# Optimization experiments

Measured on AMD Instinct MI355X. Metric: run time of the kernel, lower is better.

Reference implementation:

```python
import jax, jax.numpy as jnp
import numpy as np
from jax import lax

SCALES = [0.5, 1, 2]


def resize_bilinear_ac(x, oh, ow):
    """F.interpolate(mode='bilinear', align_corners=True) for NCHW x."""
    B, C, H, W = x.shape
    def coords(n_in, n_out):
        c = jnp.linspace(0.0, n_in - 1.0, n_out).astype(x.dtype)
        i0 = jnp.clip(jnp.floor(c).astype(jnp.int32), 0, n_in - 1)
        i1 = jnp.minimum(i0 + 1, n_in - 1)
        return i0, i1, c - i0.astype(x.dtype)
    y0, y1, wy = coords(H, oh)
    x0, x1, wx = coords(W, ow)
    top = x[:, :, y0, :] * (1 - wy)[:, None] + x[:, :, y1, :] * wy[:, None]
    return top[:, :, :, x0] * (1 - wx) + top[:, :, :, x1] * wx


def interpolate4d(t, oh, ow):
    """Geometry.interpolate4d: bilinear resize of both spatial pairs of [b,h1,w1,h2,w2]."""
    b, h1, w1, h2, w2 = t.shape
    t = t.reshape(b, h1, w1, h2 * w2).transpose(0, 3, 1, 2)
    t = resize_bilinear_ac(t, oh, ow)            # [b, h2*w2, oh, ow]
    t = t.reshape(b, h2, w2, oh * ow).transpose(0, 3, 1, 2)
    t = resize_bilinear_ac(t, oh, ow)            # [b, oh*ow, oh, ow]
    return t.reshape(b, oh, ow, oh, ow)


def conv2d_same(x, w):
    return lax.conv_general_dilated(x, w, (1, 1), [(1, 1), (1, 1)],
                                    dimension_numbers=('NCHW', 'OIHW', 'NCHW'))


def conv3d_same(x, w, p):
    return lax.conv_general_dilated(x, w, (1, 1, 1), [(p, p)] * 3,
                                    dimension_numbers=('NCDHW', 'OIDHW', 'NCDHW'))


def fast4d(corr, kernel, bias=None):
    """4D conv (stride 1, same zero-padding) via per-slice 3D convs, mirroring chm.fast4d.
    corr: [b, ci, sh, sw, th, tw]; kernel: [co, ci, k, k, k, k]."""
    b, ci, sh, sw, th, tw = corr.shape
    co, k = kernel.shape[0], kernel.shape[2]
    p = k // 2
    x = corr.transpose(0, 2, 1, 3, 4, 5).reshape(b * sh, ci, sw, th, tw)
    out = jnp.zeros((b, co, sh, sw, th, tw), corr.dtype)
    for pidx in range(k):
        ic = conv3d_same(x, kernel[:, :, pidx], p)
        ic = ic.reshape(b, sh, co, sw, th, tw).transpose(0, 2, 1, 3, 4, 5)
        a0, a1 = max(p - pidx, 0), min(sh, sh + p - pidx)
        s0, s1 = max(pidx - p, 0), min(sh, sh + pidx - p)
        out = out.at[:, :, a0:a1].add(ic[:, :, s0:s1])
    if bias is not None:
        out = out + bias.reshape(1, co, 1, 1, 1, 1)
    return out


def chm6d(corr, kernel):
    """6D conv with kernel (K,K,kk,kk,kk,kk), same zero-padding, no bias (chm.fast6d).
    corr: [b, 1, S, S, h, w, h, w]; kernel: [1, 1, K, K, kk, kk, kk, kk]."""
    b, _, S, _, h, w, _, _ = corr.shape
    K, kk = kernel.shape[2], kernel.shape[4]
    pk = K // 2
    x = corr.transpose(0, 2, 3, 1, 4, 5, 6, 7).reshape(b * S * S, 1, h, w, h, w)
    ker = kernel.reshape(1, K * K, kk, kk, kk, kk).swapaxes(0, 1)  # [K*K, 1, kk...]
    y = fast4d(x, ker).reshape(b, S, S, K * K, h, w, h, w)
    yp = jnp.pad(y, ((0, 0), (pk, pk), (pk, pk), (0, 0), (0, 0), (0, 0), (0, 0), (0, 0)))
    out = jnp.zeros((b, S, S, h, w, h, w), corr.dtype)
    for ki in range(K):
        for kj in range(K):
            out = out + yp[:, ki:ki + S, kj:kj + S, ki * K + kj]
    return out[:, None]


def mutual_nn_filter(cm):
    smax = jnp.max(cm, axis=2, keepdims=True)
    tmax = jnp.max(cm, axis=1, keepdims=True)
    smax = jnp.where(smax == 0, 1e-30, smax)
    tmax = jnp.where(tmax == 0, 1e-30, tmax)
    return cm * ((cm / smax) * (cm / tmax))


def build_correlation6d(src_feat, trg_feat, conv_ws):
    bsz, _, side, _ = src_feat.shape
    sfs, tfs = [], []
    for scale, w in zip(SCALES, conv_ws):
        s = int(np.floor(scale * side))
        sfs.append(conv2d_same(resize_bilinear_ac(src_feat, s, s), w))
        tfs.append(conv2d_same(resize_bilinear_ac(trg_feat, s, s), w))
    corr6d = []
    for sf in sfs:
        ch, ss = sf.shape[1], sf.shape[-1]
        sv = sf.reshape(bsz, ch, ss * ss).transpose(0, 2, 1)   # [b, ss^2, ch]
        sn = jnp.linalg.norm(sv, axis=2, keepdims=True)
        for tf in tfs:
            ts = tf.shape[-1]
            tv = tf.reshape(bsz, ch, ts * ts)                  # [b, ch, ts^2]
            tn = jnp.linalg.norm(tv, axis=1, keepdims=True)
            c = jnp.einsum('bsc,bct->bst', sv, tv) / (sn * tn)
            corr6d.append(interpolate4d(c.reshape(bsz, ss, ss, ts, ts), side, side))
    corr = jnp.stack(corr6d).reshape(3, 3, bsz, side, side, side, side)
    corr = corr.transpose(2, 0, 1, 3, 4, 5, 6)                 # [b, 3, 3, s, s, s, s]
    return jnp.maximum(corr, 0.0)


def chm_forward(src_feat, trg_feat, w0, w1, w2, k6, k4, b4):
    bsz, _, side, _ = src_feat.shape
    corr = build_correlation6d(src_feat, trg_feat, (w0, w1, w2))[:, None]
    corr = jax.nn.sigmoid(chm6d(corr, k6))                     # [b,1,3,3,h,w,h,w]
    h = w = side
    corr = corr.reshape(bsz, -1, h, w, h, w).max(axis=1)       # max over 9 scale pairs
    corr = interpolate4d(corr, 2 * h, 2 * w)[:, None]          # [b,1,2h,2w,2h,2w]
    corr = jax.nn.softplus(fast4d(corr, k4, b4)[:, 0])
    n = corr.shape[-1] ** 2
    return mutual_nn_filter(corr.reshape(bsz, n, n))


def setup_inputs() -> dict:
    key = jax.random.key(0)
    ks = jax.random.split(key, 8)
    b, fd, side = 4, 1024, 16
    w_std = 0.02  # ~kaiming for 3x3 conv with fan_in 1024*9
    return {
        'src_feat': jax.random.normal(ks[0], (b, fd, side, side), jnp.float32),
        'trg_feat': jax.random.normal(ks[1], (b, fd, side, side), jnp.float32),
        'conv_w0': jax.random.normal(ks[2], (fd // 4, fd, 3, 3), jnp.float32) * w_std,
        'conv_w1': jax.random.normal(ks[3], (fd // 4, fd, 3, 3), jnp.float32) * w_std,
        'conv_w2': jax.random.normal(ks[4], (fd // 4, fd, 3, 3), jnp.float32) * w_std,
        'chm6d_w': jax.random.normal(ks[5], (1, 1, 3, 3, 5, 5, 5, 5), jnp.float32) * 0.05,
        'chm4d_w': jax.random.normal(ks[6], (1, 1, 5, 5, 5, 5), jnp.float32) * 0.05,
        'chm4d_b': jnp.zeros((1,), jnp.float32),
    }


def reference(src_feat, trg_feat, conv_w0, conv_w1, conv_w2, chm6d_w, chm4d_w, chm4d_b):
    return chm_forward(src_feat, trg_feat, conv_w0, conv_w1, conv_w2, chm6d_w, chm4d_w, chm4d_b)
```

## Files before the change

kernel.cpp:

```cpp
#include <hip/hip_runtime.h>
#include <cstdint>
#include <cstddef>


#define DEVFN __device__ __forceinline__

typedef __attribute__((ext_vector_type(8))) short short8v;
typedef __attribute__((ext_vector_type(4))) float f32x4;
typedef unsigned int u32;

DEVFN void gl_lds16(const void* g, void* l){
  __builtin_amdgcn_global_load_lds(
      (const __attribute__((address_space(1))) u32*)g,
      (__attribute__((address_space(3))) u32*)l, 16, 0, 0);
}

constexpr size_t OFF_WB    = 0;
constexpr size_t OFF_P8    = 3538944;
constexpr size_t OFF_P16   = 3948544;
constexpr size_t OFF_P32   = 5275648;
constexpr size_t OFF_SF8   = 10010624;
constexpr size_t OFF_TF8   = 10076160;
constexpr size_t OFF_SF16  = 10141696;
constexpr size_t OFF_TF16  = 10403840;
constexpr size_t OFF_SF32  = 10665984;
constexpr size_t OFF_TF32  = 11714560;
constexpr size_t OFF_INVS  = 12763136;
constexpr size_t OFF_INVT  = 12768512;
constexpr size_t OFF_TMAX  = 12777984;
constexpr size_t OFF_CORR6 = 12782080;
constexpr size_t OFF_CMAXP = OFF_CORR6 + 2359296 + 128;
constexpr size_t OFF_WA    = OFF_CMAXP + 131072;
constexpr size_t OFF_PARTK = OFF_WA + 96128;
constexpr size_t OFF_SMAXP = OFF_PARTK + 2752512;
constexpr size_t OFF_WA4   = OFF_SMAXP + 16384;
constexpr size_t WS_FLOATS = OFF_WA4 + 12800;

__device__ constexpr size_t PAIR_OFF[9] = {
  OFF_WB + 0,       OFF_WB + 16384,   OFF_WB + 81920,
  OFF_WB + 344064,  OFF_WB + 409600,  OFF_WB + 671744,
  OFF_WB + 1720320, OFF_WB + 1982464, OFF_WB + 3031040 };
constexpr size_t OFF_CL    = 0;
constexpr size_t OFF_MAXED = 9437184;
constexpr size_t OFF_INT32 = 262144;
constexpr size_t OFF_FB    = OFF_PARTK;

__device__ constexpr int SSARR[3] = {8, 16, 32};
__device__ constexpr int PAIR_START[9] = {0,4,20,84,100,164,420,484,740};

DEVFN unsigned short f2bf(float f){
  unsigned int u = __float_as_uint(f);
  return (unsigned short)((u + 0x7fffu + ((u >> 16) & 1u)) >> 16);
}
DEVFN float bf2f(unsigned short u){
  return __uint_as_float(((unsigned int)u) << 16);
}

__global__ __launch_bounds__(256) void k_wpack(const float* __restrict__ w0,
                                               const float* __restrict__ w1,
                                               const float* __restrict__ w2,
                                               float* __restrict__ wsf){
  int bx = blockIdx.x;
  int scale = bx >> 8, cg = (bx >> 4) & 15, ig = bx & 15;
  const float* w = (scale==0) ? w0 : (scale==1 ? w1 : w2);
  const int t = threadIdx.x;
  __shared__ float sW[16*580];
  const float* src = w + (size_t)cg*16*9216 + (size_t)ig*576;
  for (int i=t; i<9216; i+=256){
    int co = i/576, r = i%576;
    sW[co*580 + r] = src[(size_t)co*9216 + r];
  }
  __syncthreads();
  unsigned short* ob = (unsigned short*)(wsf + OFF_WB) + (size_t)scale*2359296;
  for (int f=t; f<1152; f+=256){
    int tap = f/128, rem = f%128, kcl = rem>>6, l = rem&63;
    int kc = ig*2 + kcl;
    int co = l & 15;
    int ciL = kcl*32 + ((l>>4)&3)*8;
    unsigned short* o = ob + ((size_t)tap*32768 + (size_t)kc*1024 + (size_t)cg*64 + l)*8;
    #pragma unroll
    for (int i=0;i<8;i++)
      o[i] = f2bf(sW[co*580 + (ciL+i)*9 + tap]);
  }
}

__global__ void k_wa(const float* __restrict__ k6, float* __restrict__ wsf){
  int gid = blockIdx.x*256 + threadIdx.x;
  if (gid >= 24000) return;
  int tap = gid / 192, rem = gid % 192;
  int kc = rem / 64, l = rem % 64;
  int d = tap % 5, ac = tap / 5, a = ac / 5, c = ac % 5;
  int so = l & 15, k8 = (l >> 4) * 8;
  unsigned short* o = (unsigned short*)(wsf + OFF_WA) + (size_t)gid*8;
  #pragma unroll
  for (int i=0;i<8;i++){
    int kg = kc*32 + k8 + i;
    int e = kg >> 4, pr = kg & 15;
    float v = 0.f;
    if (so < 9 && pr < 9 && e < 5){
      int pi = pr/3, pj = pr%3, sio = so/3, sjo = so%3;
      int ki = pi - sio + 1, kj = pj - sjo + 1;
      if (ki>=0 && ki<=2 && kj>=0 && kj<=2)
        v = k6[(((((ki*3+kj)*5 + a)*5 + c)*5 + d)*5) + e];
    }
    o[i] = f2bf(v);
  }
}

__global__ void k_wa4(const float* __restrict__ k4, float* __restrict__ wsf){
  int gid = blockIdx.x*256 + threadIdx.x;
  if (gid >= 3200) return;
  int d = gid / 640, rem = gid % 640;
  int kc = rem / 64, l = rem % 64;
  int so = l & 15, soy = so >> 2, sox = so & 3;
  int e = kc >> 1;
  int pyw = 4*(kc & 1) + (l >> 4);
  unsigned short* o = (unsigned short*)(wsf + OFF_WA4) + (size_t)gid*8;
  #pragma unroll
  for (int i=0;i<8;i++){
    int a = pyw - soy, c = i - sox;
    float v = 0.f;
    if (a>=0 && a<=4 && c>=0 && c<=4)
      v = k4[((a*5 + c)*5 + d)*5 + e];
    o[i] = f2bf(v);
  }
}

__global__ __launch_bounds__(256) void k_inpack(const float* __restrict__ src,
                                                const float* __restrict__ trg,
                                                float* __restrict__ wsf){
  int bt = blockIdx.x >> 6, cg = blockIdx.x & 63;
  int chbase = cg*16;
  int t = threadIdx.x;
  __shared__ float sIn[16][257];
  const float* gin = ((bt>=4)? trg : src) + ((size_t)(bt&3)*1024 + chbase)*256;
  #pragma unroll
  for (int i=0;i<16;i++){
    int idx = t + i*256; int ch = idx>>8, pos = idx&255;
    sIn[ch][pos] = gin[(size_t)ch*256 + pos];
  }
  __syncthreads();
  int ch = t & 15, pw = t >> 4;
  #pragma unroll 1
  for (int s=0; s<3; s++){
    int S = SSARR[s], Sp = S+2, Sp2 = Sp*Sp;
    size_t poff = (s==0)?OFF_P8 : (s==1)?OFF_P16 : OFF_P32;
    unsigned short* o = (unsigned short*)(wsf + poff) + (size_t)bt*Sp2*1024 + chbase + ch;
    float rs = 15.f/(float)(S-1);
    for (int i = pw; i < Sp2; i += 16){
      int py = i / Sp, px = i % Sp;
      float v = 0.f;
      if (py>0 && py<Sp-1 && px>0 && px<Sp-1){
        float cy = (float)(py-1)*rs, cx = (float)(px-1)*rs;
        int y0 = (int)cy; if (y0>15) y0=15; int y1 = (y0+1<16)?y0+1:15; float fy = cy-(float)y0;
        int x0 = (int)cx; if (x0>15) x0=15; int x1 = (x0+1<16)?x0+1:15; float fx = cx-(float)x0;
        v = (1.f-fy)*((1.f-fx)*sIn[ch][y0*16+x0] + fx*sIn[ch][y0*16+x1])
          +       fy*((1.f-fx)*sIn[ch][y1*16+x0] + fx*sIn[ch][y1*16+x1]);
      }
      o[(size_t)i*1024] = f2bf(v);
    }
  }
}

__global__ __launch_bounds__(256) void k_conv_mfma(float* __restrict__ wsf){
  int bs = (blockIdx.x & 7)*84 + (blockIdx.x >> 3);
  const int ks = bs & 1;
  int bx = bs >> 1;
  int scale, bt, cot, post, S, lgS;
  if (bx < 256)      { scale=2; S=32; lgS=5; bt=bx>>5; cot=(bx>>4)&1; post=bx&15; }
  else if (bx < 320) { int r=bx-256; scale=1; S=16; lgS=4; bt=r>>3; cot=(r>>2)&1; post=r&3; }
  else               { int r=bx-320; scale=0; S=8;  lgS=3; bt=r>>1; cot=r&1; post=0; }
  const int Sp = S+2, N = S*S;
  const unsigned short* WbS = (const unsigned short*)(wsf + OFF_WB) + (size_t)scale*2359296;
  size_t poff = scale==0?OFF_P8: scale==1?OFF_P16:OFF_P32;
  const unsigned short* Pb = (const unsigned short*)(wsf + poff) + (size_t)bt*Sp*Sp*1024;
  size_t obase = (scale==2) ? (bt>=4?OFF_TF32:OFF_SF32)
               : (scale==1) ? (bt>=4?OFF_TF16:OFF_SF16)
                            : (bt>=4?OFF_TF8 :OFF_SF8);
  if (ks) obase += OFF_PARTK - OFF_SF8;
  float* outp = wsf + obase + (size_t)(bt&3)*256*N;

  const int t = threadIdx.x, l = t&63, w = t>>6, wm = w&1, wn = w>>1;
  const int nc_base = cot*8;
  const int pos0 = post*64;
  const int it0 = ks*72, it1 = it0 + 72;

  __shared__ __align__(16) unsigned short Ab[2][8192];
  __shared__ __align__(16) unsigned short Bb[2][4096];

  f32x4 acc[4][2];
  #pragma unroll
  for (int i=0;i<4;i++)
    #pragma unroll
    for (int j=0;j<2;j++) acc[i][j] = (f32x4){0.f,0.f,0.f,0.f};

  auto STAGE = [&](int buf, int it){
    int tap = it>>4, kq = it&15;
    int dy = tap/3, dx = tap - dy*3;
    #pragma unroll
    for (int j=0;j<4;++j){
      int c = w + j*4;
      int kc = c>>3, nc = c&7;
      const unsigned short* src =
        WbS + ((((size_t)tap*32 + kq*2 + kc)*16 + nc_base + nc)*64 + l)*8;
      gl_lds16(src, &Ab[buf][c*512]);
    }
    #pragma unroll
    for (int j=0;j<2;++j){
      int c = w + j*4;
      int kc = c>>2, np = c&3;
      int pos = pos0 + np*16 + (l&15);
      int y = pos>>lgS, x = pos&(S-1);
      int row = (y+dy)*Sp + (x+dx);
      int ci = kq*64 + kc*32 + ((l>>4)<<3);
      gl_lds16(Pb + (size_t)row*1024 + ci, &Bb[buf][c*512]);
    }
  };

  STAGE(0, it0);
  __syncthreads();
  int buf = 0;
  #pragma unroll 1
  for (int it=it0; it<it1; ++it){
    if (it+1 < it1) STAGE(buf^1, it+1);
    #pragma unroll
    for (int kc=0; kc<2; ++kc){
      short8v a0 = *(const short8v*)&Ab[buf][((kc*8 + wm*4 + 0)*64 + l)*8];
      short8v a1 = *(const short8v*)&Ab[buf][((kc*8 + wm*4 + 1)*64 + l)*8];
      short8v a2 = *(const short8v*)&Ab[buf][((kc*8 + wm*4 + 2)*64 + l)*8];
      short8v a3 = *(const short8v*)&Ab[buf][((kc*8 + wm*4 + 3)*64 + l)*8];
      short8v b0 = *(const short8v*)&Bb[buf][((kc*4 + wn*2 + 0)*64 + l)*8];
      short8v b1 = *(const short8v*)&Bb[buf][((kc*4 + wn*2 + 1)*64 + l)*8];
      acc[0][0] = __builtin_amdgcn_mfma_f32_16x16x32_bf16(a0, b0, acc[0][0], 0,0,0);
      acc[1][0] = __builtin_amdgcn_mfma_f32_16x16x32_bf16(a1, b0, acc[1][0], 0,0,0);
      acc[2][0] = __builtin_amdgcn_mfma_f32_16x16x32_bf16(a2, b0, acc[2][0], 0,0,0);
      acc[3][0] = __builtin_amdgcn_mfma_f32_16x16x32_bf16(a3, b0, acc[3][0], 0,0,0);
      acc[0][1] = __builtin_amdgcn_mfma_f32_16x16x32_bf16(a0, b1, acc[0][1], 0,0,0);
      acc[1][1] = __builtin_amdgcn_mfma_f32_16x16x32_bf16(a1, b1, acc[1][1], 0,0,0);
      acc[2][1] = __builtin_amdgcn_mfma_f32_16x16x32_bf16(a2, b1, acc[2][1], 0,0,0);
      acc[3][1] = __builtin_amdgcn_mfma_f32_16x16x32_bf16(a3, b1, acc[3][1], 0,0,0);
    }
    __syncthreads();
    buf ^= 1;
  }

  const int r0 = (l>>4)*4, cl = l&15;
  float* ob = outp + (size_t)(cot*128 + wm*64)*N + pos0 + wn*32 + cl;
  #pragma unroll
  for (int mf=0; mf<4; ++mf)
    #pragma unroll
    for (int nf=0; nf<2; ++nf){
      float* op = ob + (size_t)(mf*16 + r0)*N + nf*16;
      #pragma unroll
      for (int i=0;i<4;++i) op[(size_t)i*N] = acc[mf][nf][i];
    }
}

__global__ void k_combine(float* __restrict__ ws){
  int i = blockIdx.x*256 + threadIdx.x;
  ws[OFF_SF8 + i] += ws[OFF_PARTK + i];
}

__global__ __launch_bounds__(256) void k_fbpack(float* __restrict__ ws){
  int bx = blockIdx.x;
  int tsr = bx/84, r = bx%84;
  int s, b, chunk;
  if (r < 4)       { s=0; b=r;        chunk=0; }
  else if (r < 20) { s=1; int q=r-4;  b=q>>2; chunk=q&3; }
  else             { s=2; int q=r-20; b=q>>4; chunk=q&15; }
  int P = SSARR[s]*SSARR[s];
  size_t fbase = (s==0)? (tsr?OFF_TF8 :OFF_SF8)
               : (s==1)? (tsr?OFF_TF16:OFF_SF16)
                       : (tsr?OFF_TF32:OFF_SF32);
  const float* src = ws + fbase + (size_t)b*256*P;
  int pos0 = chunk*64;
  const int t = threadIdx.x;
  __shared__ float tile[64][260];
  for (int i=0;i<64;i++){
    int idx = t + i*256; int ch = idx>>6, pl = idx&63;
    tile[pl][ch] = src[(size_t)ch*P + pos0 + pl];
  }
  __syncthreads();
  int rowbase = tsr*5376 + (s==0?0: s==1?256:1280) + b*P + pos0;
  unsigned short* FB = (unsigned short*)(ws + OFF_FB);
  for (int i=0;i<64;i++){
    int idx = t + i*256; int pl = idx>>8, ch = idx&255;
    FB[(size_t)(rowbase+pl)*256 + ch] = f2bf(tile[pl][ch]);
  }
}

__global__ void k_invnorm(float* __restrict__ ws){
  int gid = blockIdx.x*256 + threadIdx.x;
  int row = gid >> 4, sub = gid & 15;
  const unsigned short* fb = (const unsigned short*)(ws + OFF_FB)
                           + (size_t)row*256 + sub*16;
  float s = 0.f;
  #pragma unroll
  for (int i=0;i<2;i++){
    short8v v = *(const short8v*)(fb + i*8);
    #pragma unroll
    for (int j=0;j<8;j++){
      float f = bf2f(((unsigned short*)&v)[j]);
      s = fmaf(f, f, s);
    }
  }
  #pragma unroll
  for (int m=1; m<16; m<<=1) s += __shfl_xor(s, m);
  if (sub == 0){
    int tsr = row/5376, r = row%5376;
    ws[(tsr ? OFF_INVT : OFF_INVS) + r] = 1.f/sqrtf(s);
  }
}

__global__ __launch_bounds__(256) void k_corr(float* __restrict__ ws){
  int bx = blockIdx.x;
  int p = (bx>=4)+(bx>=20)+(bx>=84)+(bx>=100)+(bx>=164)+(bx>=420)+(bx>=484)+(bx>=740);
  int si = p/3, ti = p%3;
  int M = SSARR[si]*SSARR[si], N = SSARR[ti]*SSARR[ti];
  int ntN = N >> 6;
  int rem = bx - PAIR_START[p];
  int b = rem & 3; rem >>= 2;
  int nt = rem % ntN, mt = rem / ntN;
  int m0 = mt*64, n0 = nt*64;
  const unsigned short* FB = (const unsigned short*)(ws + OFF_FB);
  const unsigned short* Ap = FB + (size_t)((si==0?0: si==1?256:1280) + b*M + m0)*256;
  const unsigned short* Bp = FB + (size_t)(5376 + (ti==0?0: ti==1?256:1280) + b*N + n0)*256;
  const int t = threadIdx.x, l = t&63, w = t>>6, wm = w&1, wn = w>>1;
  const int mrow = wm*32 + (l&15), ncol = wn*32 + (l&15);
  f32x4 acc[2][2];
  #pragma unroll
  for (int i=0;i<2;i++)
    #pragma unroll
    for (int j=0;j<2;j++) acc[i][j] = (f32x4){0.f,0.f,0.f,0.f};
  #pragma unroll
  for (int ksp=0; ksp<8; ++ksp){
    const int ko = ksp*32 + ((l>>4)&3)*8;
    short8v a0 = *(const short8v*)(Ap + (size_t) mrow     *256 + ko);
    short8v a1 = *(const short8v*)(Ap + (size_t)(mrow+16) *256 + ko);
    short8v b0 = *(const short8v*)(Bp + (size_t) ncol     *256 + ko);
    short8v b1 = *(const short8v*)(Bp + (size_t)(ncol+16) *256 + ko);
    acc[0][0] = __builtin_amdgcn_mfma_f32_16x16x32_bf16(a0, b0, acc[0][0], 0,0,0);
    acc[1][0] = __builtin_amdgcn_mfma_f32_16x16x32_bf16(a1, b0, acc[1][0], 0,0,0);
    acc[0][1] = __builtin_amdgcn_mfma_f32_16x16x32_bf16(a0, b1, acc[0][1], 0,0,0);
    acc[1][1] = __builtin_amdgcn_mfma_f32_16x16x32_bf16(a1, b1, acc[1][1], 0,0,0);
  }
  const float* iS = ws + OFF_INVS + (si==0?0: si==1?256:1280) + (size_t)b*M;
  const float* iT = ws + OFF_INVT + (ti==0?0: ti==1?256:1280) + (size_t)b*N;
  float* C = ws + PAIR_OFF[p] + (size_t)b*M*N;
  const int r0 = (l>>4)*4, cl = l&15;
  #pragma unroll
  for (int mf=0; mf<2; ++mf)
    #pragma unroll
    for (int nf=0; nf<2; ++nf)
      #pragma unroll
      for (int i=0;i<4;++i){
        int m = m0 + wm*32 + mf*16 + r0 + i;
        int n = n0 + wn*32 + nf*16 + cl;
        C[(size_t)m*N + n] = acc[mf][nf][i]*iS[m]*iT[n];
      }
}

DEVFN void cw_coord(int i, int n, int OH, int& i0, int& i1, float& f){
  float c = (float)(i*(n-1))/(float)(OH-1);
  int a = (int)c; if (a > n-1) a = n-1;
  i0 = a; i1 = (a+1 < n) ? a+1 : n-1; f = c - (float)a;
}

__global__ __launch_bounds__(256) void k_interp_pairs(float* __restrict__ ws){
  int bx = blockIdx.x;
  int p = bx >> 10;
  int bl = bx & 1023;
  int b = bl >> 8, oy = (bl >> 4) & 15, ox = bl & 15;
  int si = p/3, ti = p%3;
  int h1 = SSARR[si], t1 = SSARR[ti], t12 = t1*t1;
  int y0,y1,x0,x1; float fy,fx;
  cw_coord(oy,h1,16,y0,y1,fy); cw_coord(ox,h1,16,x0,x1,fx);
  const float* in = ws + PAIR_OFF[p] + (size_t)b*h1*h1*t12;
  __shared__ float sPl[4][1024];
  const int t = threadIdx.x;
  {
    const float* pl0 = in + (size_t)(y0*h1+x0)*t12;
    const float* pl1 = in + (size_t)(y0*h1+x1)*t12;
    const float* pl2 = in + (size_t)(y1*h1+x0)*t12;
    const float* pl3 = in + (size_t)(y1*h1+x1)*t12;
    for (int i=t; i<t12; i+=256){
      sPl[0][i] = pl0[i]; sPl[1][i] = pl1[i];
      sPl[2][i] = pl2[i]; sPl[3][i] = pl3[i];
    }
  }
  __syncthreads();
  int px = t & 15, py = t >> 4;
  int u0,u1,v0,v1; float fu,fv;
  cw_coord(py,t1,16,u0,u1,fu); cw_coord(px,t1,16,v0,v1,fv);
  float wY[2]={1.f-fy,fy}, wX[2]={1.f-fx,fx};
  float wU[2]={1.f-fu,fu}, wV[2]={1.f-fv,fv};
  int us[2]={u0,u1}, vs[2]={v0,v1};
  float s = 0.f;
  #pragma unroll
  for (int qa=0; qa<2; qa++)
    #pragma unroll
    for (int qc=0; qc<2; qc++){
      float wyx = wY[qa]*wX[qc];
      const float* base = sPl[qa*2+qc];
      #pragma unroll
      for (int qu=0; qu<2; qu++)
        #pragma unroll
        for (int qv=0; qv<2; qv++)
          s += wyx*wU[qu]*wV[qv]*base[us[qu]*t1 + vs[qv]];
    }
  ws[OFF_CORR6 + ((size_t)b*9 + p)*65536 + ((size_t)(oy*16+ox)<<8) + t] = fmaxf(s, 0.f);
}

__global__ __launch_bounds__(256) void k_cl(float* __restrict__ ws){
  int bx = blockIdx.x;
  int b = bx >> 8, yx = bx & 255;
  const int t = threadIdx.x;
  __shared__ __align__(16) unsigned short tile[10080];
  for (int i=t; i<1260; i+=256)
    *reinterpret_cast<f32x4*>((float*)&tile[i*8]) = (f32x4){0.f,0.f,0.f,0.f};
  __syncthreads();
  const float* c6 = ws + OFF_CORR6 + ((size_t)b*9 << 16) + ((size_t)yx << 8);
  const int qy = t >> 4, qx = t & 15;
  const int wo = ((2+qy)*21 + 2+qx)*24;
  #pragma unroll
  for (int pr=0; pr<9; ++pr)
    tile[wo + pr] = f2bf(c6[((size_t)pr << 16) + t]);
  __syncthreads();
  unsigned short* o = (unsigned short*)(ws + OFF_CL) + (size_t)bx*10080;
  for (int i=t; i<1260; i+=256)
    *reinterpret_cast<f32x4*>((float*)&o[i*8]) =
      *reinterpret_cast<const f32x4*>((const float*)&tile[i*8]);
}

__global__ __launch_bounds__(256) void k_chm6d(float* __restrict__ ws){
  int id = (blockIdx.x & 7)*128 + (blockIdx.x >> 3);
  const int b = id >> 8, sy = (id >> 4) & 15, sx = id & 15;
  const int t = threadIdx.x, l = t & 63, w = t >> 6;
  const int x = l & 15, h = (l >> 4) & 1, e2 = (l >> 4) >> 1;
  const unsigned short* CLu = (const unsigned short*)(ws + OFF_CL);
  const unsigned short* WAu = (const unsigned short*)(ws + OFF_WA);
  __shared__ __align__(16) unsigned short tile[2][10080];

  f32x4 acc[4];
  #pragma unroll
  for (int i=0;i<4;i++) acc[i] = (f32x4){0.f,0.f,0.f,0.f};

  auto STAGE = [&](int buf, int YX){
    const unsigned short* src = CLu + (size_t)(b*256 + YX)*10080;
    #pragma unroll
    for (int j=0;j<5;++j){
      int ch = t + j*256;
      if (ch < 1260) gl_lds16(src + (size_t)ch*8, &tile[buf][ch*8]);
    }
  };

  const int xb0 = (x + e2)*24 + 8*h;

  int i0 = 0;
  for (; i0 < 25; ++i0){
    int Y = sy + i0/5 - 2, X = sx + i0%5 - 2;
    if (Y>=0 && Y<=15 && X>=0 && X<=15) break;
  }
  {
    int Y = sy + i0/5 - 2, X = sx + i0%5 - 2;
    STAGE(0, Y*16 + X);
  }
  __syncthreads();
  int buf = 0, i = i0;
  #pragma unroll 1
  while (i < 25){
    int nx = i + 1;
    for (; nx < 25; ++nx){
      int Y = sy + nx/5 - 2, X = sx + nx%5 - 2;
      if (Y>=0 && Y<=15 && X>=0 && X<=15) break;
    }
    if (nx < 25){
      int Y = sy + nx/5 - 2, X = sx + nx%5 - 2;
      STAGE(buf^1, Y*16 + X);
    }
    {
      const unsigned short* wa = WAu + (size_t)i*5*3*512;
      short8v afr[5][3];
      #pragma unroll
      for (int d=0; d<5; ++d)
        #pragma unroll
        for (int kc=0; kc<3; ++kc)
          afr[d][kc] = *(const short8v*)&wa[((d*3 + kc)*64 + l)*8];
      const unsigned short* tb = &tile[buf][0];
      #pragma unroll
      for (int rl=0; rl<8; ++rl){
        const int row = (w*4 + rl)*504;
        short8v bf0 = *(const short8v*)&tb[row + xb0];
        short8v bf1 = *(const short8v*)&tb[row + xb0 + 48];
        short8v bf2 = *(const short8v*)&tb[row + xb0 + 96];
        #pragma unroll
        for (int y=0; y<4; ++y){
          if (y <= rl && rl - y <= 4){
            const int d = rl - y;
            acc[y] = __builtin_amdgcn_mfma_f32_16x16x32_bf16(afr[d][0], bf0, acc[y], 0,0,0);
            acc[y] = __builtin_amdgcn_mfma_f32_16x16x32_bf16(afr[d][1], bf1, acc[y], 0,0,0);
            acc[y] = __builtin_amdgcn_mfma_f32_16x16x32_bf16(afr[d][2], bf2, acc[y], 0,0,0);
          }
        }
      }
    }
    __syncthreads();
    buf ^= 1; i = nx;
  }

  const int g = l >> 4;
  float* maxed = ws + OFF_MAXED + (size_t)b*65536 + (size_t)(sy*16+sx)*256;
  #pragma unroll
  for (int y=0; y<4; ++y){
    float lm;
    if (g < 2)      lm = fmaxf(fmaxf(acc[y][0], acc[y][1]), fmaxf(acc[y][2], acc[y][3]));
    else if (g==2)  lm = acc[y][0];
    else            lm = -1e30f;
    lm = fmaxf(lm, __shfl_xor(lm, 16));
    lm = fmaxf(lm, __shfl_xor(lm, 32));
    if (l < 16)
      maxed[(w*4 + y)*16 + x] = 1.f/(1.f + expf(-lm));
  }
}

__global__ void k_interp32(float* __restrict__ ws){
  int id = blockIdx.x*256 + threadIdx.x;
  int px = id & 31, py = (id>>5)&31, ox = (id>>10)&31, oy = (id>>15)&31, b = id>>20;
  int y0,y1,x0,x1,u0,u1,v0,v1; float fy,fx,fu,fv;
  cw_coord(oy,16,32,y0,y1,fy); cw_coord(ox,16,32,x0,x1,fx);
  cw_coord(py,16,32,u0,u1,fu); cw_coord(px,16,32,v0,v1,fv);
  const float* in = ws + OFF_MAXED + (size_t)b*65536;
  int ys[2]={y0,y1}, xs[2]={x0,x1}, us[2]={u0,u1}, vs[2]={v0,v1};
  float wy[2]={1.f-fy,fy}, wx[2]={1.f-fx,fx}, wu[2]={1.f-fu,fu}, wv[2]={1.f-fv,fv};
  float s = 0.f;
  #pragma unroll
  for (int ia=0; ia<2; ia++)
    #pragma unroll
    for (int ic=0; ic<2; ic++){
      float wyx = wy[ia]*wx[ic];
      const float* base = in + ((size_t)ys[ia]*16 + xs[ic])*256;
      #pragma unroll
      for (int id_=0; id_<2; id_++)
        #pragma unroll
        for (int ie=0; ie<2; ie++)
          s += wyx*wu[id_]*wv[ie]*base[(size_t)us[id_]*16 + vs[ie]];
    }
  ws[OFF_INT32 + id] = s;
}

__global__ __launch_bounds__(256) void k_fast4d(float* __restrict__ ws,
                                                const float* __restrict__ b4,
                                                float* __restrict__ out){
  int id = (blockIdx.x & 7)*128 + (blockIdx.x >> 3);
  const int b = id >> 8, rem = id & 255;
  const int syb = rem >> 5, sxb = (rem >> 2) & 7, yh = rem & 3;
  const int t = threadIdx.x, l = t & 63, w = t >> 6;
  __shared__ __align__(16) unsigned short T[27648];
  __shared__ float red[4][16];
  for (int i=t; i<3456; i+=256)
    *reinterpret_cast<f32x4*>((float*)&T[i*8]) = (f32x4){0.f,0.f,0.f,0.f};
  __syncthreads();
  const float* I = ws + OFF_INT32 + (size_t)b*1048576;
  #pragma unroll 4
  for (int j=0; j<48; ++j){
    int idx2 = j*256 + t;
    int xo = idx2 & 15, pl = (idx2>>4) & 63, ry = idx2 >> 10;
    int pya = syb*4 + (pl>>3) - 2;
    int pxa = sxb*4 + (pl&7) - 2;
    int rya = yh*8 + ry - 2;
    if (pya>=0 && pya<32 && pxa>=0 && pxa<32 && rya>=0 && rya<32){
      float2 v = *reinterpret_cast<const float2*>(
          I + (size_t)(pya*32+pxa)*1024 + rya*32 + xo*2);
      int base = (ry*36 + xo*2 + 2)*64 + pl;
      T[base]      = f2bf(v.x);
      T[base + 64] = f2bf(v.y);
    }
  }
  __syncthreads();
  const unsigned short* WA4 = (const unsigned short*)(ws + OFF_WA4);
  f32x4 acc[2][2];
  #pragma unroll
  for (int i=0;i<2;i++)
    #pragma unroll
    for (int j=0;j<2;j++) acc[i][j] = (f32x4){0.f,0.f,0.f,0.f};
  const unsigned short* Tl = T + (l&15)*64 + (l>>4)*8 + w*2*2304;
  #pragma unroll 1
  for (int d=0; d<5; ++d){
    short8v afr[10];
    #pragma unroll
    for (int kc=0; kc<10; ++kc)
      afr[kc] = *(const short8v*)&WA4[((size_t)(d*10 + kc)*64 + l)*8];
    #pragma unroll
    for (int y2=0; y2<2; ++y2){
      const unsigned short* Tr = Tl + (y2 + d)*2304;
      #pragma unroll
      for (int xg=0; xg<2; ++xg){
        const unsigned short* Tx = Tr + xg*1024;
        #pragma unroll
        for (int kc=0; kc<10; ++kc){
          short8v bf = *(const short8v*)&Tx[(kc>>1)*64 + (kc&1)*32];
          acc[y2][xg] = __builtin_amdgcn_mfma_f32_16x16x32_bf16(afr[kc], bf, acc[y2][xg], 0,0,0);
        }
      }
    }
  }
  const float bias = b4[0];
  float rm[4] = {-1e30f,-1e30f,-1e30f,-1e30f};
  #pragma unroll
  for (int y2=0; y2<2; ++y2)
    #pragma unroll
    for (int xg=0; xg<2; ++xg)
      #pragma unroll
      for (int i=0; i<4; ++i){
        int so = (l>>4)*4 + i;
        float xv = acc[y2][xg][i] + bias;
        float sp = fmaxf(xv,0.f) + log1pf(expf(-fabsf(xv)));
        int row = (syb*4 + (so>>2))*32 + sxb*4 + (so&3);
        int col = (yh*8 + w*2 + y2)*32 + xg*16 + (l&15);
        out[((size_t)b*1024 + row)*1024 + col] = sp;
        rm[i] = fmaxf(rm[i], sp);
      }
  #pragma unroll
  for (int m=1; m<16; m<<=1)
    #pragma unroll
    for (int i=0;i<4;++i) rm[i] = fmaxf(rm[i], __shfl_xor(rm[i], m));
  if ((l & 15) == 0){
    #pragma unroll
    for (int i=0;i<4;++i) red[w][(l>>4)*4 + i] = rm[i];
  }
  __syncthreads();
  if (t < 16){
    float m = fmaxf(fmaxf(red[0][t], red[1][t]), fmaxf(red[2][t], red[3][t]));
    int row = (syb*4 + (t>>2))*32 + sxb*4 + (t&3);
    ws[OFF_SMAXP + (size_t)yh*4096 + (size_t)b*1024 + row] = m;
  }
}

__global__ void k_colmax_p(const float* __restrict__ cm, float* __restrict__ ws){
  int b = blockIdx.x >> 7, rg = (blockIdx.x >> 2) & 31, cg = blockIdx.x & 3;
  int c = cg*256 + threadIdx.x;
  const float* base = cm + (size_t)b*1048576 + (size_t)rg*32768 + c;
  float m = -1e30f;
  #pragma unroll 4
  for (int r=0; r<32; r++) m = fmaxf(m, base[(size_t)r*1024]);
  ws[OFF_CMAXP + (size_t)(b*32+rg)*1024 + c] = m;
}

__global__ void k_colmax_r(float* __restrict__ ws){
  int id = blockIdx.x*256 + threadIdx.x;
  int b = id >> 10, c = id & 1023;
  float m = -1e30f;
  #pragma unroll
  for (int rg=0; rg<32; rg++)
    m = fmaxf(m, ws[OFF_CMAXP + (size_t)(b*32+rg)*1024 + c]);
  ws[OFF_TMAX + id] = m;
}

__global__ void k_mutual(float* __restrict__ cm, const float* __restrict__ ws){
  int id = blockIdx.x*256 + threadIdx.x;
  int b = id >> 20, r = (id>>10)&1023, c = id&1023;
  float v  = cm[id];
  size_t si = (size_t)(b<<10) + r;
  float sm = fmaxf(fmaxf(ws[OFF_SMAXP + si],        ws[OFF_SMAXP + 4096 + si]),
                   fmaxf(ws[OFF_SMAXP + 8192 + si], ws[OFF_SMAXP + 12288 + si]));
  float tm = ws[OFF_TMAX + (b<<10) + c];
  sm = (sm==0.f) ? 1e-30f : sm;
  tm = (tm==0.f) ? 1e-30f : tm;
  cm[id] = v * (v/sm) * (v/tm);
}

extern "C" void kernel_launch(void* const* d_in, const int* in_sizes, int n_in,
                              void* d_out, int out_size, void* d_ws, size_t ws_size,
                              hipStream_t stream){
  const float* src = (const float*)d_in[0];
  const float* trg = (const float*)d_in[1];
  const float* w0  = (const float*)d_in[2];
  const float* w1  = (const float*)d_in[3];
  const float* w2  = (const float*)d_in[4];
  const float* k6  = (const float*)d_in[5];
  const float* k4  = (const float*)d_in[6];
  const float* b4  = (const float*)d_in[7];
  float* ws  = (float*)d_ws;
  float* out = (float*)d_out;
  (void)in_sizes; (void)n_in; (void)out_size; (void)ws_size;

  k_wpack       <<<768,   256, 0, stream>>>(w0, w1, w2, ws);
  k_wa          <<<94,    256, 0, stream>>>(k6, ws);
  k_wa4         <<<13,    256, 0, stream>>>(k4, ws);
  k_inpack      <<<512,   256, 0, stream>>>(src, trg, ws);
  k_conv_mfma   <<<672,   256, 0, stream>>>(ws);
  k_combine     <<<10752, 256, 0, stream>>>(ws);
  k_fbpack      <<<168,   256, 0, stream>>>(ws);
  k_invnorm     <<<672,   256, 0, stream>>>(ws);
  k_corr        <<<1764,  256, 0, stream>>>(ws);
  k_interp_pairs<<<9216,  256, 0, stream>>>(ws);
  k_cl          <<<1024,  256, 0, stream>>>(ws);
  k_chm6d       <<<1024,  256, 0, stream>>>(ws);
  k_interp32    <<<16384, 256, 0, stream>>>(ws);
  k_fast4d      <<<1024,  256, 0, stream>>>(ws, b4, out);
  k_colmax_p    <<<512,   256, 0, stream>>>(out, ws);
  k_colmax_r    <<<16,    256, 0, stream>>>(ws);
  k_mutual      <<<16384, 256, 0, stream>>>(out, ws);
}
```

Baseline: 377.1 us.

## Fuse split-K partial combine into fbpack and remap conv block-to-XCD schedule

Removes the standalone k_combine kernel by having k_fbpack add the split-K partial sums while it loads tiles. The packed bf16 feature buffer moves to a new workspace region, so it no longer overwrites the partial-sum area that is still being read. The conv block index mapping is also reworked so the two K-halves of a tile run adjacently on the same XCD, which should improve L2 reuse. This saves one full read/write pass over the features and one launch, and costs extra workspace.

```diff
diff --git a/kernel.cpp b/kernel.cpp
--- a/kernel.cpp
+++ b/kernel.cpp
@@ -34,7 +34,8 @@
 constexpr size_t OFF_PARTK = OFF_WA + 96128;
 constexpr size_t OFF_SMAXP = OFF_PARTK + 2752512;
 constexpr size_t OFF_WA4   = OFF_SMAXP + 16384;
-constexpr size_t WS_FLOATS = OFF_WA4 + 12800;
+constexpr size_t OFF_FB3   = OFF_WA4 + 12800;
+constexpr size_t WS_FLOATS = OFF_FB3 + 1376256;
 
 __device__ constexpr size_t PAIR_OFF[9] = {
   OFF_WB + 0,       OFF_WB + 16384,   OFF_WB + 81920,
@@ -43,7 +44,6 @@
 constexpr size_t OFF_CL    = 0;
 constexpr size_t OFF_MAXED = 9437184;
 constexpr size_t OFF_INT32 = 262144;
-constexpr size_t OFF_FB    = OFF_PARTK;
 
 __device__ constexpr int SSARR[3] = {8, 16, 32};
 __device__ constexpr int PAIR_START[9] = {0,4,20,84,100,164,420,484,740};
@@ -163,13 +163,20 @@
 }
 
 __global__ __launch_bounds__(256) void k_conv_mfma(float* __restrict__ wsf){
-  int bs = (blockIdx.x & 7)*84 + (blockIdx.x >> 3);
-  const int ks = bs & 1;
-  int bx = bs >> 1;
-  int scale, bt, cot, post, S, lgS;
-  if (bx < 256)      { scale=2; S=32; lgS=5; bt=bx>>5; cot=(bx>>4)&1; post=bx&15; }
-  else if (bx < 320) { int r=bx-256; scale=1; S=16; lgS=4; bt=r>>3; cot=(r>>2)&1; post=r&3; }
-  else               { int r=bx-320; scale=0; S=8;  lgS=3; bt=r>>1; cot=r&1; post=0; }
+  int bxid = blockIdx.x;
+  int scale, bt, cot, post, ks, S, lgS;
+  if (bxid < 512){
+    int xcd = bxid & 7, j2 = bxid >> 3;
+    int g = (j2 >> 5)*8 + xcd;
+    int j = j2 & 31;
+    scale = 2; S = 32; lgS = 5;
+    bt = g >> 1; cot = g & 1; post = j >> 1; ks = j & 1;
+  } else {
+    int r = bxid - 512;
+    ks = r & 1; int bx = 256 + (r >> 1);
+    if (bx < 320){ int q=bx-256; scale=1; S=16; lgS=4; bt=q>>3; cot=(q>>2)&1; post=q&3; }
+    else         { int q=bx-320; scale=0; S=8;  lgS=3; bt=q>>1; cot=q&1; post=0; }
+  }
   const int Sp = S+2, N = S*S;
   const unsigned short* WbS = (const unsigned short*)(wsf + OFF_WB) + (size_t)scale*2359296;
   size_t poff = scale==0?OFF_P8: scale==1?OFF_P16:OFF_P32;
@@ -256,11 +263,6 @@
     }
 }
 
-__global__ void k_combine(float* __restrict__ ws){
-  int i = blockIdx.x*256 + threadIdx.x;
-  ws[OFF_SF8 + i] += ws[OFF_PARTK + i];
-}
-
 __global__ __launch_bounds__(256) void k_fbpack(float* __restrict__ ws){
   int bx = blockIdx.x;
   int tsr = bx/84, r = bx%84;
@@ -273,16 +275,18 @@
                : (s==1)? (tsr?OFF_TF16:OFF_SF16)
                        : (tsr?OFF_TF32:OFF_SF32);
   const float* src = ws + fbase + (size_t)b*256*P;
+  const float* prt = ws + OFF_PARTK + (fbase - OFF_SF8) + (size_t)b*256*P;
   int pos0 = chunk*64;
   const int t = threadIdx.x;
   __shared__ float tile[64][260];
   for (int i=0;i<64;i++){
     int idx = t + i*256; int ch = idx>>6, pl = idx&63;
-    tile[pl][ch] = src[(size_t)ch*P + pos0 + pl];
+    size_t o = (size_t)ch*P + pos0 + pl;
+    tile[pl][ch] = src[o] + prt[o];
   }
   __syncthreads();
   int rowbase = tsr*5376 + (s==0?0: s==1?256:1280) + b*P + pos0;
-  unsigned short* FB = (unsigned short*)(ws + OFF_FB);
+  unsigned short* FB = (unsigned short*)(ws + OFF_FB3);
   for (int i=0;i<64;i++){
     int idx = t + i*256; int pl = idx>>8, ch = idx&255;
     FB[(size_t)(rowbase+pl)*256 + ch] = f2bf(tile[pl][ch]);
@@ -292,7 +296,7 @@
 __global__ void k_invnorm(float* __restrict__ ws){
   int gid = blockIdx.x*256 + threadIdx.x;
   int row = gid >> 4, sub = gid & 15;
-  const unsigned short* fb = (const unsigned short*)(ws + OFF_FB)
+  const unsigned short* fb = (const unsigned short*)(ws + OFF_FB3)
                            + (size_t)row*256 + sub*16;
   float s = 0.f;
   #pragma unroll
@@ -322,7 +326,7 @@
   int b = rem & 3; rem >>= 2;
   int nt = rem % ntN, mt = rem / ntN;
   int m0 = mt*64, n0 = nt*64;
-  const unsigned short* FB = (const unsigned short*)(ws + OFF_FB);
+  const unsigned short* FB = (const unsigned short*)(ws + OFF_FB3);
   const unsigned short* Ap = FB + (size_t)((si==0?0: si==1?256:1280) + b*M + m0)*256;
   const unsigned short* Bp = FB + (size_t)(5376 + (ti==0?0: ti==1?256:1280) + b*N + n0)*256;
   const int t = threadIdx.x, l = t&63, w = t>>6, wm = w&1, wn = w>>1;
@@ -689,7 +693,6 @@
   k_wa4         <<<13,    256, 0, stream>>>(k4, ws);
   k_inpack      <<<512,   256, 0, stream>>>(src, trg, ws);
   k_conv_mfma   <<<672,   256, 0, stream>>>(ws);
-  k_combine     <<<10752, 256, 0, stream>>>(ws);
   k_fbpack      <<<168,   256, 0, stream>>>(ws);
   k_invnorm     <<<672,   256, 0, stream>>>(ws);
   k_corr        <<<1764,  256, 0, stream>>>(ws);
```

After: 371.1 us. No clear change (-1.6%).
